# Optimization experiments

Hardware: AMD Instinct MI355X
Metric: run time of the kernel (lower is better)

## Reference

```python
import jax, jax.numpy as jnp
import numpy as np

T_LAYER = 2            # number of time chunks in this layer
T_NXT = 2              # p: number of phase-shifted spike trains emitted
THRESH = 1.0 - 0.001   # spike threshold used by catCuda.getSpikes


def avg_pool2(x):
    """2x2 spatial average pooling on [N, C, H, W, Tc] (stride 2)."""
    N, C, H, W, T = x.shape
    x = x.reshape(N, C, H // 2, 2, W // 2, 2, T)
    return x.mean(axis=(3, 5))


def get_spikes(x, th):
    """Integrate-and-fire spike generation over trailing time dim.
    v <- v + x_t; spike if v >= th; v <- v - spike*th. Same math as
    catCuda.getSpikes."""
    xt = jnp.moveaxis(x, -1, 0)  # [T, N, C, H, W]

    def step(v, xi):
        u = v + xi
        s = (u >= th).astype(x.dtype)
        return u - s * th, s

    _, s = jax.lax.scan(step, jnp.zeros_like(xt[0]), xt)
    return jnp.moveaxis(s, 0, -1)


def setup_inputs() -> dict:
    key = jax.random.key(0)
    x = jax.random.uniform(key, (16, 128, 64, 64, 8), dtype=jnp.float32)
    return {"x": x}


def reference(x):
    # chunk along time, pool each chunk spatially, average over chunks
    chunks = jnp.split(x, T_LAYER, axis=-1)
    x_out = jnp.stack([avg_pool2(c) for c in chunks]).mean(axis=0)
    # p phase-shifted spike encodings, concatenated on the time dim
    outs = [get_spikes((i * x_out) % THRESH + x_out, THRESH) for i in range(T_NXT)]
    return jnp.concatenate(outs, axis=-1)
```

## Files before the change

kernel.cpp:

```cpp
#include <hip/hip_runtime.h>


#define TH 0.999f

typedef float f4 __attribute__((ext_vector_type(4)));

__global__ __launch_bounds__(256) void spikepool_kernel(
    const float* __restrict__ x, float* __restrict__ out)
{
    const int tid = blockIdx.x * 256 + threadIdx.x;

    const int wp = tid & 15;
    const int h  = (tid >> 4) & 31;
    const int nc = tid >> 9;

    const size_t base = (size_t)nc * 32768 + (size_t)h * 1024 + (size_t)wp * 32;
    const f4* r0p = reinterpret_cast<const f4*>(x + base);
    const f4* r1p = r0p + 128;

    float a0[32], a1[32];
#pragma unroll
    for (int i = 0; i < 8; ++i)
        *reinterpret_cast<f4*>(&a0[i * 4]) = r0p[i];
#pragma unroll
    for (int i = 0; i < 8; ++i)
        *reinterpret_cast<f4*>(&a1[i * 4]) = r1p[i];

    float o[16];

#pragma unroll
    for (int p = 0; p < 2; ++p) {
        const int b = p * 16;
        float xo[4];
#pragma unroll
        for (int t = 0; t < 4; ++t) {
            float s0 = ((a0[b + t]     + a0[b + 8 + t])  + a1[b + t])     + a1[b + 8 + t];
            float s1 = ((a0[b + 4 + t] + a0[b + 12 + t]) + a1[b + 4 + t]) + a1[b + 12 + t];
            xo[t] = (s0 * 0.25f + s1 * 0.25f) * 0.5f;
        }

        {
            float v = 0.0f;
#pragma unroll
            for (int t = 0; t < 4; ++t) {
                float u = v + xo[t];
                float s = (u >= TH) ? 1.0f : 0.0f;
                o[p * 8 + t] = s;
                v = u - s * TH;
            }
        }
        {
            float v = 0.0f;
#pragma unroll
            for (int t = 0; t < 4; ++t) {
                float m  = (xo[t] >= TH) ? (xo[t] - TH) : xo[t];
                float u = v + (m + xo[t]);
                float s = (u >= TH) ? 1.0f : 0.0f;
                o[p * 8 + 4 + t] = s;
                v = u - s * TH;
            }
        }
    }

    f4* op = reinterpret_cast<f4*>(out + (size_t)tid * 16);
#pragma unroll
    for (int i = 0; i < 4; ++i) {
        f4 v = {o[i * 4], o[i * 4 + 1], o[i * 4 + 2], o[i * 4 + 3]};
        op[i] = v;
    }
}

extern "C" void kernel_launch(void* const* d_in, const int* in_sizes, int n_in,
                              void* d_out, int out_size, void* d_ws, size_t ws_size,
                              hipStream_t stream) {
    const float* x = (const float*)d_in[0];
    float* out = (float*)d_out;
    spikepool_kernel<<<4096, 256, 0, stream>>>(x, out);
}
```

Before: 75.27 us.

## Split each pooled pixel across eight lanes using f4 loads and shuffles

Each output pixel is now handled by eight cooperating lanes instead of each thread handling two whole pixels. Every lane loads one contiguous float4, and the 2x2 pooling and time-chunk averaging are done with width-8 warp shuffles; lane 0's pooled values are then broadcast to the group. Each lane computes both spike trains redundantly and writes one scalar output. The goal is more parallelism and better load coalescing for a bandwidth-bound kernel. The cost is extra shuffle instructions, redundant spike computation, and a sixteen-times larger grid.

```diff
diff --git a/kernel.cpp b/kernel.cpp
--- a/kernel.cpp
+++ b/kernel.cpp
@@ -5,69 +5,78 @@
 
 typedef float f4 __attribute__((ext_vector_type(4)));
 
+__device__ __forceinline__ f4 shfl_down4(f4 v, unsigned d) {
+    f4 r;
+    r.x = __shfl_down(v.x, d, 8);
+    r.y = __shfl_down(v.y, d, 8);
+    r.z = __shfl_down(v.z, d, 8);
+    r.w = __shfl_down(v.w, d, 8);
+    return r;
+}
+
+__device__ __forceinline__ f4 bcast4(f4 v) {
+    f4 r;
+    r.x = __shfl(v.x, 0, 8);
+    r.y = __shfl(v.y, 0, 8);
+    r.z = __shfl(v.z, 0, 8);
+    r.w = __shfl(v.w, 0, 8);
+    return r;
+}
+
 __global__ __launch_bounds__(256) void spikepool_kernel(
     const float* __restrict__ x, float* __restrict__ out)
 {
-    const int tid = blockIdx.x * 256 + threadIdx.x;
+    const int T = blockIdx.x * 256 + threadIdx.x;
+    const int j = T & 7;
+    const int P = T >> 3;
 
-    const int wp = tid & 15;
-    const int h  = (tid >> 4) & 31;
-    const int nc = tid >> 9;
+    const int w  = P & 31;
+    const int h  = (P >> 5) & 31;
+    const int nc = P >> 10;
 
-    const size_t base = (size_t)nc * 32768 + (size_t)h * 1024 + (size_t)wp * 32;
-    const f4* r0p = reinterpret_cast<const f4*>(x + base);
-    const f4* r1p = r0p + 128;
+    const size_t base = (size_t)nc * 32768 + (size_t)h * 1024 + (size_t)w * 16
+                      + (size_t)(j >> 2) * 512 + (size_t)((j >> 1) & 1) * 8
+                      + (size_t)(j & 1) * 4;
+    const f4 v = *reinterpret_cast<const f4*>(x + base);
 
-    float a0[32], a1[32];
-#pragma unroll
-    for (int i = 0; i < 8; ++i)
-        *reinterpret_cast<f4*>(&a0[i * 4]) = r0p[i];
-#pragma unroll
-    for (int i = 0; i < 8; ++i)
-        *reinterpret_cast<f4*>(&a1[i * 4]) = r1p[i];
+    f4 s = v + shfl_down4(v, 2);
+    s = s + shfl_down4(v, 4);
+    s = s + shfl_down4(v, 6);
 
-    float o[16];
+    const f4 s1 = shfl_down4(s, 1);
+    f4 xo = (s * 0.25f + s1 * 0.25f) * 0.5f;
+    xo = bcast4(xo);
 
-#pragma unroll
-    for (int p = 0; p < 2; ++p) {
-        const int b = p * 16;
-        float xo[4];
+    f4 o03;
+    {
+        float vv = 0.0f;
 #pragma unroll
         for (int t = 0; t < 4; ++t) {
-            float s0 = ((a0[b + t]     + a0[b + 8 + t])  + a1[b + t])     + a1[b + 8 + t];
-            float s1 = ((a0[b + 4 + t] + a0[b + 12 + t]) + a1[b + 4 + t]) + a1[b + 12 + t];
-            xo[t] = (s0 * 0.25f + s1 * 0.25f) * 0.5f;
+            float u = vv + xo[t];
+            float sp = (u >= TH) ? 1.0f : 0.0f;
+            o03[t] = sp;
+            vv = u - sp * TH;
         }
-
-        {
-            float v = 0.0f;
+    }
+    f4 o47;
+    {
+        float vv = 0.0f;
 #pragma unroll
-            for (int t = 0; t < 4; ++t) {
-                float u = v + xo[t];
-                float s = (u >= TH) ? 1.0f : 0.0f;
-                o[p * 8 + t] = s;
-                v = u - s * TH;
-            }
-        }
-        {
-            float v = 0.0f;
-#pragma unroll
-            for (int t = 0; t < 4; ++t) {
-                float m  = (xo[t] >= TH) ? (xo[t] - TH) : xo[t];
-                float u = v + (m + xo[t]);
-                float s = (u >= TH) ? 1.0f : 0.0f;
-                o[p * 8 + 4 + t] = s;
-                v = u - s * TH;
-            }
+        for (int t = 0; t < 4; ++t) {
+            float m  = (xo[t] >= TH) ? (xo[t] - TH) : xo[t];
+            float u  = vv + (m + xo[t]);
+            float sp = (u >= TH) ? 1.0f : 0.0f;
+            o47[t] = sp;
+            vv = u - sp * TH;
         }
     }
 
-    f4* op = reinterpret_cast<f4*>(out + (size_t)tid * 16);
-#pragma unroll
-    for (int i = 0; i < 4; ++i) {
-        f4 v = {o[i * 4], o[i * 4 + 1], o[i * 4 + 2], o[i * 4 + 3]};
-        op[i] = v;
-    }
+    const f4 tr = (j & 4) ? o47 : o03;
+    const float lohi = (j & 1) ? tr[1] : tr[0];
+    const float hihi = (j & 1) ? tr[3] : tr[2];
+    const float val  = (j & 2) ? hihi : lohi;
+
+    out[T] = val;
 }
 
 extern "C" void kernel_launch(void* const* d_in, const int* in_sizes, int n_in,
@@ -75,5 +84,5 @@
                               hipStream_t stream) {
     const float* x = (const float*)d_in[0];
     float* out = (float*)d_out;
-    spikepool_kernel<<<4096, 256, 0, stream>>>(x, out);
+    spikepool_kernel<<<65536, 256, 0, stream>>>(x, out);
 }
```

Measured after the change: 68.52 us. 1.1x faster.
